# Performance work log

Hardware: AMD Instinct MI355X
Metric: run time of the kernel (lower is better)

Reference implementation:

```python
import jax, jax.numpy as jnp
import numpy as np

B, N, C, D = 32, 4096, 16, 256

def setup_inputs() -> dict:
    key = jax.random.key(0)
    k1, k2 = jax.random.split(key)
    r_tensor = jax.random.uniform(k1, (B, N, C), dtype=jnp.float32)
    v_tensor = jax.random.normal(k2, (B, N, D), dtype=jnp.float32)
    return {"r_tensor": r_tensor, "v_tensor": v_tensor}

def reference(r_tensor, v_tensor):
    n = r_tensor.shape[1]
    mask_belong = r_tensor >= 0.5  # (B,N,C)
    # mean over N of v[:, :, None, :] * mask[..., None]  ==  mask^T @ v / N, no (B,N,C,D) intermediate
    interest_category_mean = jnp.einsum(
        'bnc,bnd->bcd', mask_belong.astype(v_tensor.dtype), v_tensor) / n  # (B,C,D)
    mask_all_below = jnp.logical_not(mask_belong).all(axis=2)  # (B,N)
    interest_special_mean = jnp.einsum(
        'bn,bnd->bd', mask_all_below.astype(v_tensor.dtype), v_tensor) / n  # (B,D)
    v_fusion = jnp.concatenate(
        [interest_category_mean, interest_special_mean[:, None, :]], axis=1)  # (B,C+1,D)
    v_fusion = jnp.where(jnp.isnan(v_fusion), jnp.zeros((), v_fusion.dtype), v_fusion)
    return v_fusion
```

## Files before the change

### kernel.cpp

```cpp
#include <hip/hip_runtime.h>

#define B_ 32
#define N_ 4096
#define C_ 16
#define D_ 256
#define NSPLIT 64
#define ROWS (N_ / NSPLIT)
#define RPW  (ROWS / 4)
#define NG   (RPW / 4)

__global__ __launch_bounds__(256, 4)
void tf_stage1(const float* __restrict__ r,
               const float* __restrict__ v,
               float* __restrict__ ws) {
    const int b     = blockIdx.x >> 6;
    const int chunk = blockIdx.x & (NSPLIT - 1);
    const int tid   = threadIdx.x;
    const int wave  = tid >> 6;
    const int lane  = tid & 63;
    const int d4    = lane << 2;

    const float* __restrict__ rb = r + (size_t)b * N_ * C_;
    const float* __restrict__ vp = v + (size_t)b * N_ * D_;

    float4 acc[17];
#pragma unroll
    for (int c = 0; c < 17; ++c) acc[c] = make_float4(0.f, 0.f, 0.f, 0.f);

    const int base = chunk * ROWS + wave * RPW;
    const float* __restrict__ rptr = rb + (size_t)base * C_ + lane;
    const float* __restrict__ vptr = vp + (size_t)base * D_ + d4;

    float  rv, rv_n;
    float4 v0, v1, v2, v3, n0, n1, n2, n3;

#define LOADG(off, RV, A, Bq, Cq, Dq)                          \
    {                                                          \
        RV = rptr[(size_t)(off) * C_];                         \
        const float* _vn = vptr + (size_t)(off) * D_;          \
        A  = *(const float4*)(_vn + 0 * D_);                   \
        Bq = *(const float4*)(_vn + 1 * D_);                   \
        Cq = *(const float4*)(_vn + 2 * D_);                   \
        Dq = *(const float4*)(_vn + 3 * D_);                   \
    }

#define ACCROW(VV, MASK)                                       \
    {                                                          \
        const unsigned _m = (MASK);                            \
        _Pragma("unroll")                                      \
        for (int c = 0; c < 16; ++c) {                         \
            const float m = (_m & (1u << c)) ? 1.0f : 0.0f;    \
            acc[c].x += (VV).x * m;                            \
            acc[c].y += (VV).y * m;                            \
            acc[c].z += (VV).z * m;                            \
            acc[c].w += (VV).w * m;                            \
        }                                                      \
        if (_m == 0u) {         \
            acc[16].x += (VV).x; acc[16].y += (VV).y;          \
            acc[16].z += (VV).z; acc[16].w += (VV).w;          \
        }                                                      \
    }

    LOADG(0, rv, v0, v1, v2, v3);

#pragma unroll
    for (int g = 0; g < NG; ++g) {
        if (g + 1 < NG) LOADG((g + 1) * 4, rv_n, n0, n1, n2, n3);

        const unsigned long long bal = __ballot(rv >= 0.5f);
        ACCROW(v0, (unsigned)(bal       ) & 0xFFFFu);
        ACCROW(v1, (unsigned)(bal >> 16 ) & 0xFFFFu);
        ACCROW(v2, (unsigned)(bal >> 32 ) & 0xFFFFu);
        ACCROW(v3, (unsigned)(bal >> 48 ) & 0xFFFFu);

        if (g + 1 < NG) { rv = rv_n; v0 = n0; v1 = n1; v2 = n2; v3 = n3; }
    }

    __shared__ float4 lds4[17 * 64];
    if (wave == 0) {
#pragma unroll
        for (int c = 0; c < 17; ++c) lds4[c * 64 + lane] = acc[c];
    }
    __syncthreads();
    for (int w = 1; w < 4; ++w) {
        if (wave == w) {
#pragma unroll
            for (int c = 0; c < 17; ++c) {
                float4 t = lds4[c * 64 + lane];
                t.x += acc[c].x; t.y += acc[c].y;
                t.z += acc[c].z; t.w += acc[c].w;
                lds4[c * 64 + lane] = t;
            }
        }
        __syncthreads();
    }

    float* __restrict__ wsb = ws + (size_t)blockIdx.x * 17 * D_;
    const float* lf = (const float*)lds4;
#pragma unroll
    for (int c = 0; c < 17; ++c) {
        wsb[c * D_ + tid] = lf[c * 256 + tid];
    }
}

__global__ __launch_bounds__(256, 8)
void tf_stage2(const float* __restrict__ ws, float* __restrict__ out) {
    const int b = blockIdx.x / 17;
    const int j = blockIdx.x % 17;
    const int d = threadIdx.x;

    const float* __restrict__ p =
        ws + ((size_t)b * NSPLIT * 17 + j) * D_ + d;
    float s = 0.0f;
#pragma unroll 8
    for (int k = 0; k < NSPLIT; ++k) s += p[(size_t)k * 17 * D_];

    out[((size_t)b * 17 + j) * D_ + d] = s * (1.0f / (float)N_);
}

extern "C" void kernel_launch(void* const* d_in, const int* in_sizes, int n_in,
                              void* d_out, int out_size, void* d_ws, size_t ws_size,
                              hipStream_t stream) {
    const float* r = (const float*)d_in[0];
    const float* v = (const float*)d_in[1];
    float* out = (float*)d_out;
    float* ws  = (float*)d_ws;

    tf_stage1<<<dim3(B_ * NSPLIT), 256, 0, stream>>>(r, v, ws);
    tf_stage2<<<dim3(B_ * 17), 256, 0, stream>>>(ws, out);
}
```

Before: 208.3 us.

## Stage v/r tiles into LDS via async global_load_lds double buffering

```diff
diff --git a/kernel.cpp b/kernel.cpp
--- a/kernel.cpp
+++ b/kernel.cpp
@@ -5,11 +5,14 @@
 #define C_ 16
 #define D_ 256
 #define NSPLIT 64
-#define ROWS (N_ / NSPLIT)
-#define RPW  (ROWS / 4)
-#define NG   (RPW / 4)
+#define ROWS   (N_ / NSPLIT)
+#define TROWS  8
+#define NTILES (ROWS / TROWS)
 
-__global__ __launch_bounds__(256, 4)
+#define AS1(p) ((const __attribute__((address_space(1))) void*)(p))
+#define AS3(p) ((__attribute__((address_space(3))) void*)(p))
+
+__global__ __launch_bounds__(256, 8)
 void tf_stage1(const float* __restrict__ r,
                const float* __restrict__ v,
                float* __restrict__ ws) {
@@ -18,89 +21,67 @@
     const int tid   = threadIdx.x;
     const int wave  = tid >> 6;
     const int lane  = tid & 63;
-    const int d4    = lane << 2;
 
     const float* __restrict__ rb = r + (size_t)b * N_ * C_;
     const float* __restrict__ vp = v + (size_t)b * N_ * D_;
+    const int base = chunk * ROWS;
 
-    float4 acc[17];
+    __shared__ float vbuf[2][TROWS * D_];
+    __shared__ float rbuf[2][TROWS * C_];
+
+    float acc[17];
 #pragma unroll
-    for (int c = 0; c < 17; ++c) acc[c] = make_float4(0.f, 0.f, 0.f, 0.f);
+    for (int c = 0; c < 17; ++c) acc[c] = 0.0f;
 
-    const int base = chunk * ROWS + wave * RPW;
-    const float* __restrict__ rptr = rb + (size_t)base * C_ + lane;
-    const float* __restrict__ vptr = vp + (size_t)base * D_ + d4;
-
-    float  rv, rv_n;
-    float4 v0, v1, v2, v3, n0, n1, n2, n3;
-
-#define LOADG(off, RV, A, Bq, Cq, Dq)                          \
-    {                                                          \
-        RV = rptr[(size_t)(off) * C_];                         \
-        const float* _vn = vptr + (size_t)(off) * D_;          \
-        A  = *(const float4*)(_vn + 0 * D_);                   \
-        Bq = *(const float4*)(_vn + 1 * D_);                   \
-        Cq = *(const float4*)(_vn + 2 * D_);                   \
-        Dq = *(const float4*)(_vn + 3 * D_);                   \
+#define STAGE_TILE(t, bf)                                                   \
+    {                                                                       \
+        const int _r0 = (t) * TROWS;                                        \
+        _Pragma("unroll")                                                   \
+        for (int _i = 0; _i < 2; ++_i) {                                    \
+            const int _row = 2 * wave + _i;                                 \
+            const float* _g =                                               \
+                vp + (size_t)(base + _r0 + _row) * D_ + lane * 4;           \
+            __builtin_amdgcn_global_load_lds(                               \
+                AS1(_g), AS3(&vbuf[bf][_row * D_]), 16, 0, 0);              \
+        }                                                                   \
+        if (wave == 0) {                                                    \
+            const float* _gr = rb + (size_t)(base + _r0) * C_ + lane;       \
+            __builtin_amdgcn_global_load_lds(                               \
+                AS1(_gr), AS3(&rbuf[bf][0]), 4, 0, 0);                      \
+            __builtin_amdgcn_global_load_lds(                               \
+                AS1(_gr + 64), AS3(&rbuf[bf][64]), 4, 0, 0);                \
+        }                                                                   \
     }
 
-#define ACCROW(VV, MASK)                                       \
-    {                                                          \
-        const unsigned _m = (MASK);                            \
-        _Pragma("unroll")                                      \
-        for (int c = 0; c < 16; ++c) {                         \
-            const float m = (_m & (1u << c)) ? 1.0f : 0.0f;    \
-            acc[c].x += (VV).x * m;                            \
-            acc[c].y += (VV).y * m;                            \
-            acc[c].z += (VV).z * m;                            \
-            acc[c].w += (VV).w * m;                            \
-        }                                                      \
-        if (_m == 0u) {         \
-            acc[16].x += (VV).x; acc[16].y += (VV).y;          \
-            acc[16].z += (VV).z; acc[16].w += (VV).w;          \
-        }                                                      \
-    }
-
-    LOADG(0, rv, v0, v1, v2, v3);
+    STAGE_TILE(0, 0);
+    __syncthreads();
 
 #pragma unroll
-    for (int g = 0; g < NG; ++g) {
-        if (g + 1 < NG) LOADG((g + 1) * 4, rv_n, n0, n1, n2, n3);
+    for (int t = 0; t < NTILES; ++t) {
+        const int cur = t & 1;
+        if (t + 1 < NTILES) STAGE_TILE(t + 1, cur ^ 1);
 
-        const unsigned long long bal = __ballot(rv >= 0.5f);
-        ACCROW(v0, (unsigned)(bal       ) & 0xFFFFu);
-        ACCROW(v1, (unsigned)(bal >> 16 ) & 0xFFFFu);
-        ACCROW(v2, (unsigned)(bal >> 32 ) & 0xFFFFu);
-        ACCROW(v3, (unsigned)(bal >> 48 ) & 0xFFFFu);
+        const unsigned long long bal0 = __ballot(rbuf[cur][lane]      >= 0.5f);
+        const unsigned long long bal1 = __ballot(rbuf[cur][64 + lane] >= 0.5f);
 
-        if (g + 1 < NG) { rv = rv_n; v0 = n0; v1 = n1; v2 = n2; v3 = n3; }
-    }
-
-    __shared__ float4 lds4[17 * 64];
-    if (wave == 0) {
 #pragma unroll
-        for (int c = 0; c < 17; ++c) lds4[c * 64 + lane] = acc[c];
-    }
-    __syncthreads();
-    for (int w = 1; w < 4; ++w) {
-        if (wave == w) {
+        for (int rr = 0; rr < TROWS; ++rr) {
+            const unsigned mm =
+                (unsigned)(((rr < 4) ? bal0 : bal1) >> (16 * (rr & 3))) & 0xFFFFu;
+            const float vv = vbuf[cur][rr * D_ + tid];
 #pragma unroll
-            for (int c = 0; c < 17; ++c) {
-                float4 t = lds4[c * 64 + lane];
-                t.x += acc[c].x; t.y += acc[c].y;
-                t.z += acc[c].z; t.w += acc[c].w;
-                lds4[c * 64 + lane] = t;
+            for (int c = 0; c < 16; ++c) {
+                const float m = (mm & (1u << c)) ? 1.0f : 0.0f;
+                acc[c] += vv * m;
             }
+            acc[16] += vv * ((mm == 0u) ? 1.0f : 0.0f);
         }
         __syncthreads();
     }
 
     float* __restrict__ wsb = ws + (size_t)blockIdx.x * 17 * D_;
-    const float* lf = (const float*)lds4;
 #pragma unroll
-    for (int c = 0; c < 17; ++c) {
-        wsb[c * D_ + tid] = lf[c * 256 + tid];
-    }
+    for (int c = 0; c < 17; ++c) wsb[c * D_ + tid] = acc[c];
 }
 
 __global__ __launch_bounds__(256, 8)
```

Measured after the change: 302.4 us. 45.2% more time.

## Halve N splits and use an 8-row register ring for deeper v prefetch

Applied to the files above, without the earlier changes.

```diff
diff --git a/kernel.cpp b/kernel.cpp
--- a/kernel.cpp
+++ b/kernel.cpp
@@ -4,16 +4,16 @@
 #define N_ 4096
 #define C_ 16
 #define D_ 256
-#define NSPLIT 64
+#define NSPLIT 32
 #define ROWS (N_ / NSPLIT)
 #define RPW  (ROWS / 4)
-#define NG   (RPW / 4)
+#define NGRP (RPW / 4)
 
 __global__ __launch_bounds__(256, 4)
 void tf_stage1(const float* __restrict__ r,
                const float* __restrict__ v,
                float* __restrict__ ws) {
-    const int b     = blockIdx.x >> 6;
+    const int b     = blockIdx.x >> 5;
     const int chunk = blockIdx.x & (NSPLIT - 1);
     const int tid   = threadIdx.x;
     const int wave  = tid >> 6;
@@ -31,18 +31,12 @@
     const float* __restrict__ rptr = rb + (size_t)base * C_ + lane;
     const float* __restrict__ vptr = vp + (size_t)base * D_ + d4;
 
-    float  rv, rv_n;
-    float4 v0, v1, v2, v3, n0, n1, n2, n3;
-
-#define LOADG(off, RV, A, Bq, Cq, Dq)                          \
-    {                                                          \
-        RV = rptr[(size_t)(off) * C_];                         \
-        const float* _vn = vptr + (size_t)(off) * D_;          \
-        A  = *(const float4*)(_vn + 0 * D_);                   \
-        Bq = *(const float4*)(_vn + 1 * D_);                   \
-        Cq = *(const float4*)(_vn + 2 * D_);                   \
-        Dq = *(const float4*)(_vn + 3 * D_);                   \
-    }
+    float rv0 = rptr[0];
+    float rv1 = rptr[64];
+    float4 ring[8];
+#pragma unroll
+    for (int s = 0; s < 8; ++s)
+        ring[s] = *(const float4*)(vptr + (size_t)s * D_);
 
 #define ACCROW(VV, MASK)                                       \
     {                                                          \
@@ -55,25 +49,29 @@
             acc[c].z += (VV).z * m;                            \
             acc[c].w += (VV).w * m;                            \
         }                                                      \
-        if (_m == 0u) {         \
-            acc[16].x += (VV).x; acc[16].y += (VV).y;          \
-            acc[16].z += (VV).z; acc[16].w += (VV).w;          \
-        }                                                      \
+        const float ms = (_m == 0u) ? 1.0f : 0.0f;             \
+        acc[16].x += (VV).x * ms; acc[16].y += (VV).y * ms;    \
+        acc[16].z += (VV).z * ms; acc[16].w += (VV).w * ms;    \
     }
 
-    LOADG(0, rv, v0, v1, v2, v3);
-
 #pragma unroll
-    for (int g = 0; g < NG; ++g) {
-        if (g + 1 < NG) LOADG((g + 1) * 4, rv_n, n0, n1, n2, n3);
-
-        const unsigned long long bal = __ballot(rv >= 0.5f);
-        ACCROW(v0, (unsigned)(bal       ) & 0xFFFFu);
-        ACCROW(v1, (unsigned)(bal >> 16 ) & 0xFFFFu);
-        ACCROW(v2, (unsigned)(bal >> 32 ) & 0xFFFFu);
-        ACCROW(v3, (unsigned)(bal >> 48 ) & 0xFFFFu);
-
-        if (g + 1 < NG) { rv = rv_n; v0 = n0; v1 = n1; v2 = n2; v3 = n3; }
+    for (int g = 0; g < NGRP; ++g) {
+        const float rvc = (g & 1) ? rv1 : rv0;
+        const unsigned long long bal = __ballot(rvc >= 0.5f);
+        if (g + 2 < NGRP) {
+            const float rnew = rptr[(size_t)(g + 2) * 64];
+            if (g & 1) rv1 = rnew; else rv0 = rnew;
+        }
+#pragma unroll
+        for (int rr = 0; rr < 4; ++rr) {
+            const int row  = 4 * g + rr;
+            const int slot = row & 7;
+            const float4 vv = ring[slot];
+            if (row + 8 < RPW)
+                ring[slot] = *(const float4*)(vptr + (size_t)(row + 8) * D_);
+            const unsigned mm = (unsigned)(bal >> (16 * rr)) & 0xFFFFu;
+            ACCROW(vv, mm);
+        }
     }
 
     __shared__ float4 lds4[17 * 64];
```

Measured after the change: 201.5 us. -3.3%, faster.
